# Kernel optimization log

Measured on AMD Instinct MI355X. Metric: run time of the kernel, lower is better.

## Reference

```python
import jax, jax.numpy as jnp
import numpy as np

# Config (matches init_kwargs)
B, S = 2, 2048            # 2 packed sequences of 2048 tokens (prefill)
HQ, HK, D = 32, 8, 128    # GQA: 32 query heads, 8 kv heads
G = HQ // HK              # group size 4
WINDOW = 1024             # sliding window
THETA = 10000.0


def setup_inputs() -> dict:
    key = jax.random.key(0)
    kq, kk, kv = jax.random.split(key, 3)
    n_tokens = B * S
    query = jax.random.normal(kq, (n_tokens, HQ * D), dtype=jnp.float32)
    key_t = jax.random.normal(kk, (n_tokens, HK * D), dtype=jnp.float32)
    value = jax.random.normal(kv, (n_tokens, HK * D), dtype=jnp.float32)
    # per-sequence positions restart at 0 for each packed sequence
    positions = jnp.tile(jnp.arange(S, dtype=jnp.int32), B)
    return {"query": query, "key": key_t, "value": value, "positions": positions}


def _rope(x, positions):
    # x: [B, S, H, D]; rotate-half (NeoX) RoPE
    half = D // 2
    inv_freq = 1.0 / (THETA ** (jnp.arange(0, half, dtype=jnp.float32) / half))
    ang = positions.astype(jnp.float32)[:, None] * inv_freq[None, :]   # [B*S, D/2]
    cos = jnp.cos(ang).reshape(B, S, 1, half)
    sin = jnp.sin(ang).reshape(B, S, 1, half)
    x1, x2 = x[..., :half], x[..., half:]
    return jnp.concatenate([x1 * cos - x2 * sin, x2 * cos + x1 * sin], axis=-1)


def reference(query, key, value, positions):
    q = query.reshape(B, S, HQ, D)
    k = key.reshape(B, S, HK, D)
    v = value.reshape(B, S, HK, D)
    q = _rope(q, positions)
    k = _rope(k, positions)
    # GQA: split q heads into [HK, G]
    qg = q.reshape(B, S, HK, G, D)
    scale = 1.0 / jnp.sqrt(jnp.float32(D))
    # scores: [B, HK, G, Sq, Skv]
    scores = jnp.einsum('bqhgd,bshd->bhgqs', qg, k) * scale
    i = jnp.arange(S)[:, None]
    j = jnp.arange(S)[None, :]
    # causal + sliding window: j <= i and i - j < WINDOW
    mask = (j <= i) & ((i - j) < WINDOW)
    scores = jnp.where(mask[None, None, None], scores, jnp.float32(-1e30))
    attn = jax.nn.softmax(scores, axis=-1)
    out = jnp.einsum('bhgqs,bshd->bqhgd', attn, v)   # [B, Sq, HK, G, D]
    return out.reshape(B * S, HQ * D)
```

## Files before the change

kernel.cpp:

```cpp
#include <hip/hip_runtime.h>
#include <stdint.h>

#define NB 2
#define NS 2048
#define NHK 8
#define ND 128
#define NWIN 1024

using bf16x8 = __bf16 __attribute__((ext_vector_type(8)));
using f32x4  = float  __attribute__((ext_vector_type(4)));
using f32x2  = float  __attribute__((ext_vector_type(2)));
using f32x8  = float  __attribute__((ext_vector_type(8)));
using u16x8  = unsigned short __attribute__((ext_vector_type(8)));
using u32x4  = unsigned int   __attribute__((ext_vector_type(4)));

#define L2_10K (13.287712379549449f / 64.0f)
#define MASKV (-3.0e38f)

static __device__ __forceinline__ float ex2(float x) {
  return __builtin_amdgcn_exp2f(x);
}

static __device__ __forceinline__ unsigned short f2bf(float x) {
  unsigned int u = __builtin_bit_cast(unsigned int, x);
  u += 0x7FFFu + ((u >> 16) & 1u);
  return (unsigned short)(u >> 16);
}

static __device__ __forceinline__ unsigned int cvtpk(float lo, float hi) {
  unsigned int r;
  asm("v_cvt_pk_bf16_f32 %0, %1, %2" : "=v"(r) : "v"(lo), "v"(hi));
  return r;
}

static __device__ __forceinline__ void gll16(const void* g, void* l) {
  __builtin_amdgcn_global_load_lds(
      (const __attribute__((address_space(1))) void*)g,
      (__attribute__((address_space(3))) void*)l, 16, 0, 0);
}

#define MFMA16(a, b, c) __builtin_amdgcn_mfma_f32_16x16x32_bf16((a), (b), (c), 0, 0, 0)

__global__ __launch_bounds__(64) void build_tab(float* __restrict__ tab) {
  const int p = blockIdx.x, f = threadIdx.x;
  float s, c;
  __sincosf((float)p * ex2(-(float)f * L2_10K), &s, &c);
  tab[(size_t)p * 128 + f] = c;
  tab[(size_t)p * 128 + 64 + f] = s;
}

__global__ __launch_bounds__(256) void prepass(
    const float* __restrict__ kin, const float* __restrict__ vin,
    const int* __restrict__ pos, const float* __restrict__ tab,
    unsigned short* __restrict__ kimg, unsigned short* __restrict__ vimg) {
  const int bid = blockIdx.x;
  const int ti = bid & 63, gidx = bid >> 6;
  const int hk = gidx & 7, b = gidx >> 3;
  const int t = threadIdx.x;

  unsigned short* kout = kimg + (size_t)bid * 4096;
#pragma unroll
  for (int uu = 0; uu < 2; ++uu) {
    const int u = t * 2 + uu;
    const int j = u >> 4;
    const int d0 = ((u & 15) << 3) ^ ((j & 7) << 3);
    const int tok = (b << 11) + (ti << 5) + j;
    const float* kp = kin + (size_t)tok * (NHK * ND) + hk * ND;
    f32x8 a = *(const f32x8*)(kp + d0);
    f32x8 p = *(const f32x8*)(kp + (d0 ^ 64));
    const float* tr = tab + (size_t)(pos[tok] & 2047) * 128 + (d0 & 63);
    f32x8 c8 = *(const f32x8*)tr;
    f32x8 s8 = *(const f32x8*)(tr + 64);
    u16x8 o;
#pragma unroll
    for (int i = 0; i < 8; ++i) {
      float val = (d0 < 64) ? (a[i] * c8[i] - p[i] * s8[i])
                            : (a[i] * c8[i] + p[i] * s8[i]);
      o[i] = f2bf(val);
    }
    *(u16x8*)(kout + (size_t)u * 8) = o;
  }

  unsigned short* vout = vimg + (size_t)bid * 4096;
  {
    const int d0 = (t >> 2) << 1;
    const int kp4 = t & 3;
    const int tok0 = (b << 11) + (ti << 5) + (kp4 << 3);
    const float* vp = vin + (size_t)tok0 * (NHK * ND) + hk * ND + d0;
    u16x8 lo, hi;
#pragma unroll
    for (int i = 0; i < 8; ++i) {
      f32x2 r = *(const f32x2*)(vp + (size_t)i * (NHK * ND));
      lo[i] = f2bf(r[0]);
      hi[i] = f2bf(r[1]);
    }
    const int sub = kp4 ^ ((d0 >> 1) & 3);
    *(u16x8*)(vout + d0 * 32 + sub * 8) = lo;
    *(u16x8*)(vout + (d0 + 1) * 32 + sub * 8) = hi;
  }
}

template <bool PRE>
__global__ __launch_bounds__(256, 3) void attn_fwd(
    const float* __restrict__ qin, const float* __restrict__ kin,
    const float* __restrict__ vin, const int* __restrict__ pos,
    const char* __restrict__ kimg, const char* __restrict__ vimg,
    const float* __restrict__ tab, float* __restrict__ out) {
  __shared__ __align__(16) char Kb[2][8192];
  __shared__ __align__(16) char Vb[2][8192];

  const int B = blockIdx.x;
  const int xcd = B & 7;
  const int i96 = B >> 3;
  const int group = xcd + ((i96 >= 48) ? 8 : 0);
  const int unit = (i96 >= 48) ? i96 - 48 : i96;
  const int hk = group & 7, b = group >> 3;
  const int isPair = unit < 16;
  const int qtA = isPair ? unit : unit + 16;
  const int qtB = 31 - unit;

  const int tid = threadIdx.x;
  const int w = tid >> 6, lane = tid & 63, h = lane >> 4, ln = lane & 15;
  const int g = w;

  const size_t gbase = (size_t)group * 64 * 8192;
  const char* kg = PRE ? kimg + gbase + (size_t)(w * 128 + lane) * 16 : nullptr;
  const char* vg = PRE ? vimg + gbase + (size_t)(w * 128 + lane) * 16 : nullptr;

  auto stage = [&](int sl, int ti) {
    if constexpr (PRE) {
      const char* ksrc = kg + (size_t)ti * 8192;
      const char* vsrc = vg + (size_t)ti * 8192;
      char* kd = &Kb[sl][w * 2048];
      char* vd = &Vb[sl][w * 2048];
      gll16(ksrc, kd);
      gll16(ksrc + 1024, kd + 1024);
      gll16(vsrc, vd);
      gll16(vsrc + 1024, vd + 1024);
    } else {
      const int j = tid >> 3;
      const int du = (tid & 7) << 4;
      const int tok = (b << 11) + (ti << 5) + j;
      const float* kp = kin + (size_t)tok * (NHK * ND) + hk * ND;
      const float pj = (float)pos[tok];
#pragma unroll
      for (int gq = 0; gq < 2; ++gq) {
        const int dd = du + gq * 8;
        f32x8 a = *(const f32x8*)(kp + dd);
        f32x8 p = *(const f32x8*)(kp + (dd ^ 64));
        u16x8 o;
#pragma unroll
        for (int i = 0; i < 8; ++i) {
          float s, c;
          __sincosf(pj * ex2(-(float)((dd & 63) + i) * L2_10K), &s, &c);
          float val = (dd < 64) ? (a[i] * c - p[i] * s) : (a[i] * c + p[i] * s);
          o[i] = f2bf(val);
        }
        *(u16x8*)(&Kb[sl][((j << 8) + (dd << 1)) ^ ((j & 7) << 4)]) = o;
      }
      const int d0 = (tid >> 2) << 1;
      const int kp4 = tid & 3;
      const float* vp = vin + (size_t)((b << 11) + (ti << 5) + (kp4 << 3)) * (NHK * ND) + hk * ND + d0;
      u16x8 lov, hiv;
#pragma unroll
      for (int i = 0; i < 8; ++i) {
        f32x2 r = *(const f32x2*)(vp + (size_t)i * (NHK * ND));
        lov[i] = f2bf(r[0]);
        hiv[i] = f2bf(r[1]);
      }
      const int sub = kp4 ^ ((d0 >> 1) & 3);
      unsigned short* vb16 = (unsigned short*)Vb[sl];
      *(u16x8*)(vb16 + d0 * 32 + sub * 8) = lov;
      *(u16x8*)(vb16 + (d0 + 1) * 32 + sub * 8) = hiv;
    }
  };

  const float QSC = 0.08838834764831845f * 1.4426950408889634f;
  const int sw = (ln & 7) << 4;
  const int vsub = (h ^ ((ln >> 1) & 3)) << 4;

#pragma unroll 1
  for (int seg = 0; seg < 2; ++seg) {
    if (seg == 1 && !isPair) break;
    const int qt = seg ? qtB : qtA;
    const int q0b = qt << 5;
    int lo = q0b - (NWIN - 1);
    if (lo < 0) lo = 0;
    lo &= ~31;
    const int ti0 = lo >> 5;
    const int nt = (q0b >> 5) - ti0 + 1;

    __syncthreads();
    stage(0, ti0);

    bf16x8 qfr[2][4];
#pragma unroll
    for (int hf = 0; hf < 2; ++hf) {
      const int qrow = q0b + hf * 16 + ln;
      const size_t tokq = (size_t)(b << 11) + qrow;
      const float* qp = qin + tokq * 4096 + (hk * 4 + g) * 128;
      const int posq = pos[tokq] & 2047;
#pragma unroll
      for (int pp = 0; pp < 2; ++pp) {
        const int rr = (pp << 5) + (h << 3);
        f32x8 lo8 = *(const f32x8*)(qp + rr);
        f32x8 hi8 = *(const f32x8*)(qp + rr + 64);
        f32x8 cc, ss;
        if constexpr (PRE) {
          const float* tp = tab + (size_t)posq * 128 + rr;
          cc = *(const f32x8*)tp;
          ss = *(const f32x8*)(tp + 64);
        } else {
          const float pf = (float)posq;
#pragma unroll
          for (int i = 0; i < 8; ++i) {
            float s, c;
            __sincosf(pf * ex2(-(float)(rr + i) * L2_10K), &s, &c);
            cc[i] = c;
            ss[i] = s;
          }
        }
        u16x8 ulo, uhi;
#pragma unroll
        for (int i = 0; i < 8; ++i) {
          ulo[i] = f2bf((lo8[i] * cc[i] - hi8[i] * ss[i]) * QSC);
          uhi[i] = f2bf((hi8[i] * cc[i] + lo8[i] * ss[i]) * QSC);
        }
        qfr[hf][pp] = __builtin_bit_cast(bf16x8, ulo);
        qfr[hf][2 + pp] = __builtin_bit_cast(bf16x8, uhi);
      }
    }

    f32x4 Oc[2][8] = {};
    float msh[2] = {-1e30f, -1e30f};
    float lsum[2] = {};

#pragma unroll 1
    for (int t = 0; t < nt; ++t) {
      asm volatile("s_waitcnt vmcnt(0)" ::: "memory");
      __syncthreads();
      if (t + 1 < nt) stage((t + 1) & 1, ti0 + t + 1);

      const int j0 = (ti0 + t) << 5;
      const char* KB = Kb[t & 1];

      f32x4 sT[2][2] = {};
      __builtin_amdgcn_s_setprio(1);
#pragma unroll
      for (int c = 0; c < 4; ++c) {
        const bf16x8 k0 = *(const bf16x8*)(
            KB + (((ln << 8) + (c << 6) + (h << 4)) ^ sw));
        const bf16x8 k1 = *(const bf16x8*)(
            KB + ((((16 + ln) << 8) + (c << 6) + (h << 4)) ^ sw));
        sT[0][0] = MFMA16(k0, qfr[0][c], sT[0][0]);
        sT[0][1] = MFMA16(k1, qfr[0][c], sT[0][1]);
        sT[1][0] = MFMA16(k0, qfr[1][c], sT[1][0]);
        sT[1][1] = MFMA16(k1, qfr[1][c], sT[1][1]);
      }
      __builtin_amdgcn_s_setprio(0);

      if ((j0 >= q0b) || (j0 < q0b - 992)) {
#pragma unroll
        for (int qh = 0; qh < 2; ++qh) {
          const int irow = q0b + qh * 16 + ln;
#pragma unroll
          for (int ki = 0; ki < 2; ++ki)
#pragma unroll
            for (int r = 0; r < 4; ++r) {
              const int j = j0 + ki * 16 + (h << 2) + r;
              if (!(j <= irow && irow - j < NWIN)) sT[qh][ki][r] = MASKV;
            }
        }
      }

      float pm[2];
#pragma unroll
      for (int qh = 0; qh < 2; ++qh) {
        const f32x4 a0 = sT[qh][0], a1 = sT[qh][1];
        pm[qh] = fmaxf(fmaxf(fmaxf(a0[0], a0[1]), fmaxf(a0[2], a0[3])),
                       fmaxf(fmaxf(a1[0], a1[1]), fmaxf(a1[2], a1[3])));
      }
      const float ov = fmaxf(pm[0] - msh[0], pm[1] - msh[1]);
      if (__any(ov > 8.0f)) {
#pragma unroll
        for (int qh = 0; qh < 2; ++qh) {
          float M = pm[qh];
          M = fmaxf(M, __shfl_xor(M, 16));
          M = fmaxf(M, __shfl_xor(M, 32));
          const float mn = fmaxf(msh[qh], M);
          const float co = ex2(msh[qh] - mn);
          msh[qh] = mn;
          lsum[qh] *= co;
          float coO[4];
#pragma unroll
          for (int r = 0; r < 4; ++r) coO[r] = __shfl(co, (h << 2) + r);
#pragma unroll
          for (int db = 0; db < 8; ++db)
#pragma unroll
            for (int r = 0; r < 4; ++r) Oc[qh][db][r] *= coO[r];
        }
      }

      bf16x8 pa[2];
#pragma unroll
      for (int qh = 0; qh < 2; ++qh) {
#pragma unroll
        for (int ki = 0; ki < 2; ++ki)
#pragma unroll
          for (int r = 0; r < 4; ++r)
            sT[qh][ki][r] = ex2(sT[qh][ki][r] - msh[qh]);
        lsum[qh] += ((sT[qh][0][0] + sT[qh][0][1]) + (sT[qh][0][2] + sT[qh][0][3])) +
                    ((sT[qh][1][0] + sT[qh][1][1]) + (sT[qh][1][2] + sT[qh][1][3]));
        unsigned int A = cvtpk(sT[qh][0][0], sT[qh][0][1]);
        unsigned int Bk = cvtpk(sT[qh][0][2], sT[qh][0][3]);
        unsigned int C = cvtpk(sT[qh][1][0], sT[qh][1][1]);
        unsigned int D = cvtpk(sT[qh][1][2], sT[qh][1][3]);
        asm volatile("v_permlane32_swap_b32 %0, %1" : "+v"(A), "+v"(C));
        asm volatile("v_permlane16_swap_b32 %0, %1" : "+v"(A), "+v"(C));
        asm volatile("v_permlane32_swap_b32 %0, %1" : "+v"(Bk), "+v"(D));
        asm volatile("v_permlane16_swap_b32 %0, %1" : "+v"(Bk), "+v"(D));
        u32x4 pk4 = {A, Bk, C, D};
        pa[qh] = __builtin_bit_cast(bf16x8, pk4);
      }

      const char* VB = Vb[t & 1];
      __builtin_amdgcn_s_setprio(1);
#pragma unroll
      for (int db = 0; db < 8; ++db) {
        const bf16x8 vv = *(const bf16x8*)(VB + (db << 10) + (ln << 6) + vsub);
        Oc[0][db] = MFMA16(pa[0], vv, Oc[0][db]);
        Oc[1][db] = MFMA16(pa[1], vv, Oc[1][db]);
      }
      __builtin_amdgcn_s_setprio(0);
    }

#pragma unroll
    for (int qh = 0; qh < 2; ++qh) {
      float ls = lsum[qh];
      ls += __shfl_xor(ls, 16);
      ls += __shfl_xor(ls, 32);
#pragma unroll
      for (int r = 0; r < 4; ++r) {
        const float rl = 1.0f / __shfl(ls, (h << 2) + r);
        const int irow = q0b + qh * 16 + (h << 2) + r;
        float* op = out + ((size_t)(b << 11) + irow) * 4096 + (hk * 4 + g) * 128 + ln;
#pragma unroll
        for (int db = 0; db < 8; ++db) op[db * 16] = Oc[qh][db][r] * rl;
      }
    }
  }
}

extern "C" void kernel_launch(void* const* d_in, const int* in_sizes, int n_in,
                              void* d_out, int out_size, void* d_ws, size_t ws_size,
                              hipStream_t stream) {
  const float* q = (const float*)d_in[0];
  const float* k = (const float*)d_in[1];
  const float* v = (const float*)d_in[2];
  const int* pos = (const int*)d_in[3];
  float* out = (float*)d_out;

  const size_t TAB = (size_t)2048 * 128 * 4;
  const size_t KIMG = (size_t)16 * 64 * 8192;
  const size_t need = TAB + 2 * KIMG;

  if (ws_size >= need) {
    float* tab = (float*)d_ws;
    char* kimg = (char*)d_ws + TAB;
    char* vimg = kimg + KIMG;
    build_tab<<<2048, 64, 0, stream>>>(tab);
    prepass<<<1024, 256, 0, stream>>>(k, v, pos, tab,
                                      (unsigned short*)kimg, (unsigned short*)vimg);
    attn_fwd<true><<<768, 256, 0, stream>>>(q, k, v, pos, kimg, vimg, tab, out);
  } else {
    attn_fwd<false><<<768, 256, 0, stream>>>(q, k, v, pos, nullptr, nullptr, nullptr, out);
  }
}
```

Measured before the change: 95.13 us.

## Use 8-wave blocks with one 16-row query half per wave, drop tile pairing

Measured after the change: 107.2 us. 1.13x slower.

```diff
diff --git a/kernel.cpp b/kernel.cpp
--- a/kernel.cpp
+++ b/kernel.cpp
@@ -101,7 +101,7 @@
 }
 
 template <bool PRE>
-__global__ __launch_bounds__(256, 3) void attn_fwd(
+__global__ __launch_bounds__(512, 4) void attn_fwd(
     const float* __restrict__ qin, const float* __restrict__ kin,
     const float* __restrict__ vin, const int* __restrict__ pos,
     const char* __restrict__ kimg, const char* __restrict__ vimg,
@@ -110,244 +110,193 @@
   __shared__ __align__(16) char Vb[2][8192];
 
   const int B = blockIdx.x;
-  const int xcd = B & 7;
-  const int i96 = B >> 3;
-  const int group = xcd + ((i96 >= 48) ? 8 : 0);
-  const int unit = (i96 >= 48) ? i96 - 48 : i96;
+  const int group = (B & 7) + ((B >> 9) << 3);
+  const int qt = 63 - ((B >> 3) & 63);
   const int hk = group & 7, b = group >> 3;
-  const int isPair = unit < 16;
-  const int qtA = isPair ? unit : unit + 16;
-  const int qtB = 31 - unit;
 
   const int tid = threadIdx.x;
   const int w = tid >> 6, lane = tid & 63, h = lane >> 4, ln = lane & 15;
-  const int g = w;
+  const int g = w & 3, qh = w >> 2;
+  const int q0b = qt << 5;
+  const int q0 = q0b + (qh << 4);
+  int lo = q0b - (NWIN - 1);
+  if (lo < 0) lo = 0;
+  lo &= ~31;
+  const int ti0 = lo >> 5;
+  const int nt = (q0b >> 5) - ti0 + 1;
 
   const size_t gbase = (size_t)group * 64 * 8192;
-  const char* kg = PRE ? kimg + gbase + (size_t)(w * 128 + lane) * 16 : nullptr;
-  const char* vg = PRE ? vimg + gbase + (size_t)(w * 128 + lane) * 16 : nullptr;
+  const char* kg = PRE ? kimg + gbase + (size_t)tid * 16 : nullptr;
+  const char* vg = PRE ? vimg + gbase + (size_t)tid * 16 : nullptr;
 
   auto stage = [&](int sl, int ti) {
     if constexpr (PRE) {
-      const char* ksrc = kg + (size_t)ti * 8192;
-      const char* vsrc = vg + (size_t)ti * 8192;
-      char* kd = &Kb[sl][w * 2048];
-      char* vd = &Vb[sl][w * 2048];
-      gll16(ksrc, kd);
-      gll16(ksrc + 1024, kd + 1024);
-      gll16(vsrc, vd);
-      gll16(vsrc + 1024, vd + 1024);
+      gll16(kg + (size_t)ti * 8192, &Kb[sl][(w << 10)]);
+      gll16(vg + (size_t)ti * 8192, &Vb[sl][(w << 10)]);
     } else {
-      const int j = tid >> 3;
-      const int du = (tid & 7) << 4;
+      const int j = tid >> 4;
+      const int dd = (tid & 15) << 3;
       const int tok = (b << 11) + (ti << 5) + j;
       const float* kp = kin + (size_t)tok * (NHK * ND) + hk * ND;
       const float pj = (float)pos[tok];
-#pragma unroll
-      for (int gq = 0; gq < 2; ++gq) {
-        const int dd = du + gq * 8;
-        f32x8 a = *(const f32x8*)(kp + dd);
-        f32x8 p = *(const f32x8*)(kp + (dd ^ 64));
-        u16x8 o;
+      f32x8 a = *(const f32x8*)(kp + dd);
+      f32x8 p = *(const f32x8*)(kp + (dd ^ 64));
+      u16x8 o;
+#pragma unroll
+      for (int i = 0; i < 8; ++i) {
+        float s, c;
+        __sincosf(pj * ex2(-(float)((dd & 63) + i) * L2_10K), &s, &c);
+        float val = (dd < 64) ? (a[i] * c - p[i] * s) : (a[i] * c + p[i] * s);
+        o[i] = f2bf(val);
+      }
+      *(u16x8*)(&Kb[sl][((j << 8) + (dd << 1)) ^ ((j & 7) << 4)]) = o;
+      const int d = tid >> 2;
+      const int kp4 = tid & 3;
+      const float* vp = vin + (size_t)((b << 11) + (ti << 5) + (kp4 << 3)) * (NHK * ND) + hk * ND + d;
+      u16x8 ov;
+#pragma unroll
+      for (int i = 0; i < 8; ++i) ov[i] = f2bf(vp[(size_t)i * (NHK * ND)]);
+      const int sub = kp4 ^ ((d >> 1) & 3);
+      *(u16x8*)(((unsigned short*)Vb[sl]) + d * 32 + sub * 8) = ov;
+    }
+  };
+
+  stage(0, ti0);
+
+  const float QSC = 0.08838834764831845f * 1.4426950408889634f;
+  bf16x8 qfr[4];
+  {
+    const int qrow = q0 + ln;
+    const size_t tokq = (size_t)(b << 11) + qrow;
+    const float* qp = qin + tokq * 4096 + (hk * 4 + g) * 128;
+    const int posq = pos[tokq] & 2047;
+#pragma unroll
+    for (int pp = 0; pp < 2; ++pp) {
+      const int rr = (pp << 5) + (h << 3);
+      f32x8 lo8 = *(const f32x8*)(qp + rr);
+      f32x8 hi8 = *(const f32x8*)(qp + rr + 64);
+      f32x8 cc, ss;
+      if constexpr (PRE) {
+        const float* tp = tab + (size_t)posq * 128 + rr;
+        cc = *(const f32x8*)tp;
+        ss = *(const f32x8*)(tp + 64);
+      } else {
+        const float pf = (float)posq;
 #pragma unroll
         for (int i = 0; i < 8; ++i) {
           float s, c;
-          __sincosf(pj * ex2(-(float)((dd & 63) + i) * L2_10K), &s, &c);
-          float val = (dd < 64) ? (a[i] * c - p[i] * s) : (a[i] * c + p[i] * s);
-          o[i] = f2bf(val);
+          __sincosf(pf * ex2(-(float)(rr + i) * L2_10K), &s, &c);
+          cc[i] = c;
+          ss[i] = s;
         }
-        *(u16x8*)(&Kb[sl][((j << 8) + (dd << 1)) ^ ((j & 7) << 4)]) = o;
       }
-      const int d0 = (tid >> 2) << 1;
-      const int kp4 = tid & 3;
-      const float* vp = vin + (size_t)((b << 11) + (ti << 5) + (kp4 << 3)) * (NHK * ND) + hk * ND + d0;
-      u16x8 lov, hiv;
+      u16x8 ulo, uhi;
 #pragma unroll
       for (int i = 0; i < 8; ++i) {
-        f32x2 r = *(const f32x2*)(vp + (size_t)i * (NHK * ND));
-        lov[i] = f2bf(r[0]);
-        hiv[i] = f2bf(r[1]);
+        ulo[i] = f2bf((lo8[i] * cc[i] - hi8[i] * ss[i]) * QSC);
+        uhi[i] = f2bf((hi8[i] * cc[i] + lo8[i] * ss[i]) * QSC);
       }
-      const int sub = kp4 ^ ((d0 >> 1) & 3);
-      unsigned short* vb16 = (unsigned short*)Vb[sl];
-      *(u16x8*)(vb16 + d0 * 32 + sub * 8) = lov;
-      *(u16x8*)(vb16 + (d0 + 1) * 32 + sub * 8) = hiv;
-    }
-  };
-
-  const float QSC = 0.08838834764831845f * 1.4426950408889634f;
+      qfr[pp] = __builtin_bit_cast(bf16x8, ulo);
+      qfr[2 + pp] = __builtin_bit_cast(bf16x8, uhi);
+    }
+  }
+
+  f32x4 Oc[8] = {};
+  float msh = -1e30f;
+  float lsum = 0.0f;
   const int sw = (ln & 7) << 4;
   const int vsub = (h ^ ((ln >> 1) & 3)) << 4;
 
-#pragma unroll 1
-  for (int seg = 0; seg < 2; ++seg) {
-    if (seg == 1 && !isPair) break;
-    const int qt = seg ? qtB : qtA;
-    const int q0b = qt << 5;
-    int lo = q0b - (NWIN - 1);
-    if (lo < 0) lo = 0;
-    lo &= ~31;
-    const int ti0 = lo >> 5;
-    const int nt = (q0b >> 5) - ti0 + 1;
-
+  for (int t = 0; t < nt; ++t) {
+    asm volatile("s_waitcnt vmcnt(0)" ::: "memory");
     __syncthreads();
-    stage(0, ti0);
-
-    bf16x8 qfr[2][4];
-#pragma unroll
-    for (int hf = 0; hf < 2; ++hf) {
-      const int qrow = q0b + hf * 16 + ln;
-      const size_t tokq = (size_t)(b << 11) + qrow;
-      const float* qp = qin + tokq * 4096 + (hk * 4 + g) * 128;
-      const int posq = pos[tokq] & 2047;
-#pragma unroll
-      for (int pp = 0; pp < 2; ++pp) {
-        const int rr = (pp << 5) + (h << 3);
-        f32x8 lo8 = *(const f32x8*)(qp + rr);
-        f32x8 hi8 = *(const f32x8*)(qp + rr + 64);
-        f32x8 cc, ss;
-        if constexpr (PRE) {
-          const float* tp = tab + (size_t)posq * 128 + rr;
-          cc = *(const f32x8*)tp;
-          ss = *(const f32x8*)(tp + 64);
-        } else {
-          const float pf = (float)posq;
-#pragma unroll
-          for (int i = 0; i < 8; ++i) {
-            float s, c;
-            __sincosf(pf * ex2(-(float)(rr + i) * L2_10K), &s, &c);
-            cc[i] = c;
-            ss[i] = s;
-          }
+    if (t + 1 < nt) stage((t + 1) & 1, ti0 + t + 1);
+
+    const int j0 = (ti0 + t) << 5;
+    const char* KB = Kb[t & 1];
+
+    f32x4 sT[2] = {};
+    __builtin_amdgcn_s_setprio(1);
+#pragma unroll
+    for (int c = 0; c < 4; ++c) {
+      const bf16x8 k0 = *(const bf16x8*)(
+          KB + (((ln << 8) + (c << 6) + (h << 4)) ^ sw));
+      const bf16x8 k1 = *(const bf16x8*)(
+          KB + ((((16 + ln) << 8) + (c << 6) + (h << 4)) ^ sw));
+      sT[0] = MFMA16(k0, qfr[c], sT[0]);
+      sT[1] = MFMA16(k1, qfr[c], sT[1]);
+    }
+    __builtin_amdgcn_s_setprio(0);
+
+    if ((j0 >= q0b) || (j0 < q0b - 992)) {
+      const int irow = q0 + ln;
+#pragma unroll
+      for (int ki = 0; ki < 2; ++ki)
+#pragma unroll
+        for (int r = 0; r < 4; ++r) {
+          const int j = j0 + ki * 16 + (h << 2) + r;
+          if (!(j <= irow && irow - j < NWIN)) sT[ki][r] = MASKV;
         }
-        u16x8 ulo, uhi;
-#pragma unroll
-        for (int i = 0; i < 8; ++i) {
-          ulo[i] = f2bf((lo8[i] * cc[i] - hi8[i] * ss[i]) * QSC);
-          uhi[i] = f2bf((hi8[i] * cc[i] + lo8[i] * ss[i]) * QSC);
-        }
-        qfr[hf][pp] = __builtin_bit_cast(bf16x8, ulo);
-        qfr[hf][2 + pp] = __builtin_bit_cast(bf16x8, uhi);
-      }
-    }
-
-    f32x4 Oc[2][8] = {};
-    float msh[2] = {-1e30f, -1e30f};
-    float lsum[2] = {};
-
-#pragma unroll 1
-    for (int t = 0; t < nt; ++t) {
-      asm volatile("s_waitcnt vmcnt(0)" ::: "memory");
-      __syncthreads();
-      if (t + 1 < nt) stage((t + 1) & 1, ti0 + t + 1);
-
-      const int j0 = (ti0 + t) << 5;
-      const char* KB = Kb[t & 1];
-
-      f32x4 sT[2][2] = {};
-      __builtin_amdgcn_s_setprio(1);
-#pragma unroll
-      for (int c = 0; c < 4; ++c) {
-        const bf16x8 k0 = *(const bf16x8*)(
-            KB + (((ln << 8) + (c << 6) + (h << 4)) ^ sw));
-        const bf16x8 k1 = *(const bf16x8*)(
-            KB + ((((16 + ln) << 8) + (c << 6) + (h << 4)) ^ sw));
-        sT[0][0] = MFMA16(k0, qfr[0][c], sT[0][0]);
-        sT[0][1] = MFMA16(k1, qfr[0][c], sT[0][1]);
-        sT[1][0] = MFMA16(k0, qfr[1][c], sT[1][0]);
-        sT[1][1] = MFMA16(k1, qfr[1][c], sT[1][1]);
-      }
-      __builtin_amdgcn_s_setprio(0);
-
-      if ((j0 >= q0b) || (j0 < q0b - 992)) {
-#pragma unroll
-        for (int qh = 0; qh < 2; ++qh) {
-          const int irow = q0b + qh * 16 + ln;
-#pragma unroll
-          for (int ki = 0; ki < 2; ++ki)
-#pragma unroll
-            for (int r = 0; r < 4; ++r) {
-              const int j = j0 + ki * 16 + (h << 2) + r;
-              if (!(j <= irow && irow - j < NWIN)) sT[qh][ki][r] = MASKV;
-            }
-        }
-      }
-
-      float pm[2];
-#pragma unroll
-      for (int qh = 0; qh < 2; ++qh) {
-        const f32x4 a0 = sT[qh][0], a1 = sT[qh][1];
-        pm[qh] = fmaxf(fmaxf(fmaxf(a0[0], a0[1]), fmaxf(a0[2], a0[3])),
-                       fmaxf(fmaxf(a1[0], a1[1]), fmaxf(a1[2], a1[3])));
-      }
-      const float ov = fmaxf(pm[0] - msh[0], pm[1] - msh[1]);
-      if (__any(ov > 8.0f)) {
-#pragma unroll
-        for (int qh = 0; qh < 2; ++qh) {
-          float M = pm[qh];
-          M = fmaxf(M, __shfl_xor(M, 16));
-          M = fmaxf(M, __shfl_xor(M, 32));
-          const float mn = fmaxf(msh[qh], M);
-          const float co = ex2(msh[qh] - mn);
-          msh[qh] = mn;
-          lsum[qh] *= co;
-          float coO[4];
-#pragma unroll
-          for (int r = 0; r < 4; ++r) coO[r] = __shfl(co, (h << 2) + r);
-#pragma unroll
-          for (int db = 0; db < 8; ++db)
-#pragma unroll
-            for (int r = 0; r < 4; ++r) Oc[qh][db][r] *= coO[r];
-        }
-      }
-
-      bf16x8 pa[2];
-#pragma unroll
-      for (int qh = 0; qh < 2; ++qh) {
-#pragma unroll
-        for (int ki = 0; ki < 2; ++ki)
-#pragma unroll
-          for (int r = 0; r < 4; ++r)
-            sT[qh][ki][r] = ex2(sT[qh][ki][r] - msh[qh]);
-        lsum[qh] += ((sT[qh][0][0] + sT[qh][0][1]) + (sT[qh][0][2] + sT[qh][0][3])) +
-                    ((sT[qh][1][0] + sT[qh][1][1]) + (sT[qh][1][2] + sT[qh][1][3]));
-        unsigned int A = cvtpk(sT[qh][0][0], sT[qh][0][1]);
-        unsigned int Bk = cvtpk(sT[qh][0][2], sT[qh][0][3]);
-        unsigned int C = cvtpk(sT[qh][1][0], sT[qh][1][1]);
-        unsigned int D = cvtpk(sT[qh][1][2], sT[qh][1][3]);
-        asm volatile("v_permlane32_swap_b32 %0, %1" : "+v"(A), "+v"(C));
-        asm volatile("v_permlane16_swap_b32 %0, %1" : "+v"(A), "+v"(C));
-        asm volatile("v_permlane32_swap_b32 %0, %1" : "+v"(Bk), "+v"(D));
-        asm volatile("v_permlane16_swap_b32 %0, %1" : "+v"(Bk), "+v"(D));
-        u32x4 pk4 = {A, Bk, C, D};
-        pa[qh] = __builtin_bit_cast(bf16x8, pk4);
-      }
-
-      const char* VB = Vb[t & 1];
-      __builtin_amdgcn_s_setprio(1);
-#pragma unroll
-      for (int db = 0; db < 8; ++db) {
-        const bf16x8 vv = *(const bf16x8*)(VB + (db << 10) + (ln << 6) + vsub);
-        Oc[0][db] = MFMA16(pa[0], vv, Oc[0][db]);
-        Oc[1][db] = MFMA16(pa[1], vv, Oc[1][db]);
-      }
-      __builtin_amdgcn_s_setprio(0);
-    }
-
-#pragma unroll
-    for (int qh = 0; qh < 2; ++qh) {
-      float ls = lsum[qh];
-      ls += __shfl_xor(ls, 16);
-      ls += __shfl_xor(ls, 32);
-#pragma unroll
-      for (int r = 0; r < 4; ++r) {
-        const float rl = 1.0f / __shfl(ls, (h << 2) + r);
-        const int irow = q0b + qh * 16 + (h << 2) + r;
-        float* op = out + ((size_t)(b << 11) + irow) * 4096 + (hk * 4 + g) * 128 + ln;
-#pragma unroll
-        for (int db = 0; db < 8; ++db) op[db * 16] = Oc[qh][db][r] * rl;
-      }
-    }
+    }
+
+    const f32x4 a0 = sT[0], a1 = sT[1];
+    const float pm = fmaxf(fmaxf(fmaxf(a0[0], a0[1]), fmaxf(a0[2], a0[3])),
+                           fmaxf(fmaxf(a1[0], a1[1]), fmaxf(a1[2], a1[3])));
+    if (__any(pm - msh > 8.0f)) {
+      float M = pm;
+      M = fmaxf(M, __shfl_xor(M, 16));
+      M = fmaxf(M, __shfl_xor(M, 32));
+      const float mn = fmaxf(msh, M);
+      const float co = ex2(msh - mn);
+      msh = mn;
+      lsum *= co;
+      float coO[4];
+#pragma unroll
+      for (int r = 0; r < 4; ++r) coO[r] = __shfl(co, (h << 2) + r);
+#pragma unroll
+      for (int db = 0; db < 8; ++db)
+#pragma unroll
+        for (int r = 0; r < 4; ++r) Oc[db][r] *= coO[r];
+    }
+
+#pragma unroll
+    for (int ki = 0; ki < 2; ++ki)
+#pragma unroll
+      for (int r = 0; r < 4; ++r)
+        sT[ki][r] = ex2(sT[ki][r] - msh);
+    lsum += ((sT[0][0] + sT[0][1]) + (sT[0][2] + sT[0][3])) +
+            ((sT[1][0] + sT[1][1]) + (sT[1][2] + sT[1][3]));
+    unsigned int A = cvtpk(sT[0][0], sT[0][1]);
+    unsigned int Bk = cvtpk(sT[0][2], sT[0][3]);
+    unsigned int C = cvtpk(sT[1][0], sT[1][1]);
+    unsigned int D = cvtpk(sT[1][2], sT[1][3]);
+    asm volatile("v_permlane32_swap_b32 %0, %1" : "+v"(A), "+v"(C));
+    asm volatile("v_permlane16_swap_b32 %0, %1" : "+v"(A), "+v"(C));
+    asm volatile("v_permlane32_swap_b32 %0, %1" : "+v"(Bk), "+v"(D));
+    asm volatile("v_permlane16_swap_b32 %0, %1" : "+v"(Bk), "+v"(D));
+    u32x4 pk4 = {A, Bk, C, D};
+    const bf16x8 pa = __builtin_bit_cast(bf16x8, pk4);
+
+    const char* VB = Vb[t & 1];
+    __builtin_amdgcn_s_setprio(1);
+#pragma unroll
+    for (int db = 0; db < 8; ++db) {
+      const bf16x8 vv = *(const bf16x8*)(VB + (db << 10) + (ln << 6) + vsub);
+      Oc[db] = MFMA16(pa, vv, Oc[db]);
+    }
+    __builtin_amdgcn_s_setprio(0);
+  }
+
+  float ls = lsum;
+  ls += __shfl_xor(ls, 16);
+  ls += __shfl_xor(ls, 32);
+#pragma unroll
+  for (int r = 0; r < 4; ++r) {
+    const float rl = 1.0f / __shfl(ls, (h << 2) + r);
+    const int irow = q0 + (h << 2) + r;
+    float* op = out + ((size_t)(b << 11) + irow) * 4096 + (hk * 4 + g) * 128 + ln;
+#pragma unroll
+    for (int db = 0; db < 8; ++db) op[db * 16] = Oc[db][r] * rl;
   }
 }
 
@@ -371,8 +320,8 @@
     build_tab<<<2048, 64, 0, stream>>>(tab);
     prepass<<<1024, 256, 0, stream>>>(k, v, pos, tab,
                                       (unsigned short*)kimg, (unsigned short*)vimg);
-    attn_fwd<true><<<768, 256, 0, stream>>>(q, k, v, pos, kimg, vimg, tab, out);
+    attn_fwd<true><<<1024, 512, 0, stream>>>(q, k, v, pos, kimg, vimg, tab, out);
   } else {
-    attn_fwd<false><<<768, 256, 0, stream>>>(q, k, v, pos, nullptr, nullptr, nullptr, out);
-  }
-}
+    attn_fwd<false><<<1024, 512, 0, stream>>>(q, k, v, pos, nullptr, nullptr, nullptr, out);
+  }
+}
```
